# Performance work log

Hardware: AMD Instinct MI355X
Metric: run time of the kernel (lower is better)

## Reference

```python
import jax, jax.numpy as jnp
import numpy as np

NUM_HEADS = 12
DIM = 768


def setup_inputs() -> dict:
    key = jax.random.key(0)
    ks = jax.random.split(key, 7)
    B, S, E = 8, 1024, DIM
    s = 0.02
    return {
        "x": jax.random.normal(ks[0], (B, S, E), dtype=jnp.float32),
        "Wq": jax.random.normal(ks[1], (E, E), dtype=jnp.float32) * s,
        "bq": jnp.zeros((E,), dtype=jnp.float32),
        "Wk": jax.random.normal(ks[2], (E, E), dtype=jnp.float32) * s,
        "bk": jnp.zeros((E,), dtype=jnp.float32),
        "Wo": jax.random.normal(ks[3], (E, E), dtype=jnp.float32) * s,
        "bo": jnp.zeros((E,), dtype=jnp.float32),
    }


def reference(x, Wq, bq, Wk, bk, Wo, bo):
    B, S, E = x.shape
    n = NUM_HEADS
    d = E // n
    scale = d ** (-0.5)

    def heads(t):  # [B,S,E] -> [B,n,S,d]
        return t.reshape(B, S, n, d).transpose(0, 2, 1, 3)

    q = heads(x @ Wq.T + bq)
    k = heads(x @ Wk.T + bk)
    v = k  # faithful to source bug: v = self.k_w(x)

    attn = jnp.einsum('bnqd,bnkd->bnqk', q, k) * scale  # [B,n,S,S]
    attn = jax.nn.softmax(attn, axis=-1)
    out = jnp.einsum('bnqk,bnkd->bnqd', attn, v)  # [B,n,S,d]
    out = out.transpose(0, 2, 1, 3).reshape(B, S, E)
    return out @ Wo.T + bo
```

## Files before the change

### kernel.cpp

```cpp
#include <hip/hip_runtime.h>
#include <stdint.h>


using short8   = __attribute__((ext_vector_type(8))) short;
using uint4v   = __attribute__((ext_vector_type(4))) unsigned;
using float4v  = __attribute__((ext_vector_type(4))) float;
using float16v = __attribute__((ext_vector_type(16))) float;

struct __align__(8) U2 { unsigned x, y; };

__device__ __forceinline__ void async16(void* lds, const void* g) {
  __builtin_amdgcn_global_load_lds(
      (const __attribute__((address_space(1))) void*)g,
      (__attribute__((address_space(3))) void*)lds, 16, 0, 0);
}

#define LGKM_WAIT  asm volatile("s_waitcnt lgkmcnt(0)" ::: "memory")
#define BARRIER    asm volatile("s_barrier" ::: "memory")

__device__ __forceinline__ unsigned bf16b(float f) {
  union { float f; unsigned u; } v; v.f = f;
  unsigned r = v.u + 0x7FFFu + ((v.u >> 16) & 1u);
  return r >> 16;
}
__device__ __forceinline__ unsigned rne_adj(float f) {
  union { float f; unsigned u; } v; v.f = f;
  return v.u + 0x7FFFu + ((v.u >> 16) & 1u);
}
__device__ __forceinline__ unsigned pack_hi16(unsigned a, unsigned b) {
  return __builtin_amdgcn_perm(a, b, 0x07060302u);
}

__global__ __launch_bounds__(256) void cvt_bf16(const float* __restrict__ in,
                                                unsigned short* __restrict__ out,
                                                int n8) {
  int i = blockIdx.x * 256 + threadIdx.x;
  if (i >= n8) return;
  const float4v* p = (const float4v*)in;
  float4v a = p[i * 2], b = p[i * 2 + 1];
  uint4v w;
  w[0] = pack_hi16(rne_adj(a[1]), rne_adj(a[0]));
  w[1] = pack_hi16(rne_adj(a[3]), rne_adj(a[2]));
  w[2] = pack_hi16(rne_adj(b[1]), rne_adj(b[0]));
  w[3] = pack_hi16(rne_adj(b[3]), rne_adj(b[2]));
  ((uint4v*)out)[i] = w;
}

__global__ __launch_bounds__(256) void cvt_w3(const float* __restrict__ w0,
                                              const float* __restrict__ w1,
                                              const float* __restrict__ w2,
                                              unsigned short* __restrict__ o0,
                                              unsigned short* __restrict__ o1,
                                              unsigned short* __restrict__ o2) {
  int mi = blockIdx.x / 288;
  int i = (blockIdx.x - mi * 288) * 256 + threadIdx.x;
  const float* in = (mi == 0) ? w0 : (mi == 1) ? w1 : w2;
  unsigned short* out = (mi == 0) ? o0 : (mi == 1) ? o1 : o2;
  const float4v* p = (const float4v*)in;
  float4v a = p[i * 2], b = p[i * 2 + 1];
  uint4v w;
  w[0] = pack_hi16(rne_adj(a[1]), rne_adj(a[0]));
  w[1] = pack_hi16(rne_adj(a[3]), rne_adj(a[2]));
  w[2] = pack_hi16(rne_adj(b[1]), rne_adj(b[0]));
  w[3] = pack_hi16(rne_adj(b[3]), rne_adj(b[2]));
  ((uint4v*)out)[i] = w;
}

__global__ __launch_bounds__(256, 3) void sgemm_qk(
    const unsigned short* __restrict__ A, const unsigned short* __restrict__ B,
    const float* __restrict__ bias0, const float* __restrict__ bias1,
    unsigned short* __restrict__ outq, unsigned short* __restrict__ outk,
    unsigned short* __restrict__ outkt) {
  __shared__ __align__(16) unsigned short a_l[8192];
  __shared__ __align__(16) unsigned short b_l[8192];
  const int tid = threadIdx.x;
  const int w = tid >> 6, lane = tid & 63;
  const int Q4 = lane >> 4, r = lane & 15;
  const int m0 = blockIdx.x * 128;
  const int n0 = blockIdx.y * 128;
  const int wm = w >> 1, wn = w & 1;

  float4v acc[4][4];
#pragma unroll
  for (int i = 0; i < 4; ++i)
#pragma unroll
    for (int j = 0; j < 4; ++j)
#pragma unroll
      for (int g = 0; g < 4; ++g) acc[i][j][g] = 0.0f;

  const unsigned short* Ab = A + (size_t)(m0 + r) * 768 + Q4 * 8;
  const unsigned short* Bb = B + (size_t)(n0 + r) * 768 + Q4 * 8;

  uint4v ra[4], rb[4];
  auto gload = [&](int kt) {
#pragma unroll
    for (int ci = 0; ci < 4; ++ci) {
      int idx = w * 4 + ci, c = idx >> 1, kh = idx & 1;
      ra[ci] = *(const uint4v*)(Ab + c * 12288 + kt + kh * 32);
      rb[ci] = *(const uint4v*)(Bb + c * 12288 + kt + kh * 32);
    }
  };
  auto swrite = [&]() {
#pragma unroll
    for (int ci = 0; ci < 4; ++ci) {
      int idx = w * 4 + ci;
      *(uint4v*)&a_l[idx * 512 + lane * 8] = ra[ci];
      *(uint4v*)&b_l[idx * 512 + lane * 8] = rb[ci];
    }
  };

  short8 af[4][2], bf[4][2];
  auto loadf = [&]() {
#pragma unroll
    for (int i = 0; i < 4; ++i)
#pragma unroll
      for (int ks = 0; ks < 2; ++ks) {
        af[i][ks] = *(const short8*)&a_l[((wm * 4 + i) * 2 + ks) * 512 + lane * 8];
        bf[i][ks] = *(const short8*)&b_l[((wn * 4 + i) * 2 + ks) * 512 + lane * 8];
      }
  };
  auto dot = [&]() {
#pragma unroll
    for (int mt = 0; mt < 4; ++mt)
#pragma unroll
      for (int nt = 0; nt < 4; ++nt)
#pragma unroll
        for (int ks = 0; ks < 2; ++ks)
          acc[mt][nt] = __builtin_amdgcn_mfma_f32_16x16x32_bf16(
              af[mt][ks], bf[nt][ks], acc[mt][nt], 0, 0, 0);
  };

  gload(0);
#pragma unroll 1
  for (int t = 0; t < 12; ++t) {
    if (t > 0) BARRIER;
    swrite();
    if (t < 11) gload(t * 64 + 64);
    LGKM_WAIT;
    BARRIER;
    loadf();
    dot();
  }

  const bool isq = (n0 < 768);
  const float* bias = isq ? bias0 : bias1;
  unsigned short* outp = isq ? outq : outk;
  const int nb = isq ? n0 : (n0 - 768);
  const float scl = isq ? 0.18033688011112042f : 1.0f;
#pragma unroll
  for (int nt = 0; nt < 4; ++nt) {
    int n = nb + wn * 64 + nt * 16 + r;
    float bv = bias[n];
#pragma unroll
    for (int mt = 0; mt < 4; ++mt) {
      int m = m0 + wm * 64 + mt * 16 + Q4 * 4;
#pragma unroll
      for (int g = 0; g < 4; ++g)
        outp[(size_t)(m + g) * 768 + n] = (unsigned short)bf16b((acc[mt][nt][g] + bv) * scl);
    }
  }
  if (!isq) {
    const int bq = m0 >> 10;
    const int sbase = (m0 & 1023) + wm * 64 + (Q4 & 1) * 8 + (Q4 >> 1) * 4;
#pragma unroll
    for (int nt = 0; nt < 4; ++nt) {
      int n = nb + wn * 64 + nt * 16 + r;
      int hh = n >> 6, dd = n & 63;
      float bv = bias[n];
#pragma unroll
      for (int mt = 0; mt < 4; ++mt) {
        int ns = sbase + mt * 16;
        unsigned lo = pack_hi16(rne_adj(acc[mt][nt][1] + bv), rne_adj(acc[mt][nt][0] + bv));
        unsigned hi = pack_hi16(rne_adj(acc[mt][nt][3] + bv), rne_adj(acc[mt][nt][2] + bv));
        *(U2*)(outkt + (size_t)((bq * 12 + hh) * 64 + dd) * 1024 + ns) = U2{lo, hi};
      }
    }
  }
}

__global__ __launch_bounds__(256, 3) void sgemm_out(
    const unsigned short* __restrict__ A, const unsigned short* __restrict__ B,
    const float* __restrict__ bias, float* __restrict__ outp) {
  __shared__ __align__(16) unsigned short a_l[4096];
  __shared__ __align__(16) unsigned short b_l[8192];
  const int tid = threadIdx.x;
  const int w = tid >> 6, lane = tid & 63;
  const int Q4 = lane >> 4, r = lane & 15;
  const int m0 = blockIdx.y * 64;
  const int n0 = blockIdx.x * 128;
  const int wm = w >> 1, wn = w & 1;

  float4v acc[2][4];
#pragma unroll
  for (int i = 0; i < 2; ++i)
#pragma unroll
    for (int j = 0; j < 4; ++j)
#pragma unroll
      for (int g = 0; g < 4; ++g) acc[i][j][g] = 0.0f;

  const unsigned short* Ab = A + (size_t)(m0 + r) * 768 + Q4 * 8;
  const unsigned short* Bb = B + (size_t)(n0 + r) * 768 + Q4 * 8;

  uint4v ra[2], rb[4];
  auto gload = [&](int kt) {
#pragma unroll
    for (int ci = 0; ci < 2; ++ci) {
      int idx = w * 2 + ci;
      ra[ci] = *(const uint4v*)(Ab + (idx >> 1) * 12288 + kt + (idx & 1) * 32);
    }
#pragma unroll
    for (int ci = 0; ci < 4; ++ci) {
      int idx = w * 4 + ci;
      rb[ci] = *(const uint4v*)(Bb + (idx >> 1) * 12288 + kt + (idx & 1) * 32);
    }
  };
  auto swrite = [&]() {
#pragma unroll
    for (int ci = 0; ci < 2; ++ci) {
      int idx = w * 2 + ci;
      *(uint4v*)&a_l[idx * 512 + lane * 8] = ra[ci];
    }
#pragma unroll
    for (int ci = 0; ci < 4; ++ci) {
      int idx = w * 4 + ci;
      *(uint4v*)&b_l[idx * 512 + lane * 8] = rb[ci];
    }
  };

  short8 af[2][2], bf[4][2];
  auto loadf = [&]() {
#pragma unroll
    for (int i = 0; i < 2; ++i)
#pragma unroll
      for (int ks = 0; ks < 2; ++ks)
        af[i][ks] = *(const short8*)&a_l[((wm * 2 + i) * 2 + ks) * 512 + lane * 8];
#pragma unroll
    for (int i = 0; i < 4; ++i)
#pragma unroll
      for (int ks = 0; ks < 2; ++ks)
        bf[i][ks] = *(const short8*)&b_l[((wn * 4 + i) * 2 + ks) * 512 + lane * 8];
  };
  auto dot = [&]() {
#pragma unroll
    for (int mt = 0; mt < 2; ++mt)
#pragma unroll
      for (int nt = 0; nt < 4; ++nt)
#pragma unroll
        for (int ks = 0; ks < 2; ++ks)
          acc[mt][nt] = __builtin_amdgcn_mfma_f32_16x16x32_bf16(
              af[mt][ks], bf[nt][ks], acc[mt][nt], 0, 0, 0);
  };

  gload(0);
#pragma unroll 1
  for (int t = 0; t < 12; ++t) {
    if (t > 0) BARRIER;
    swrite();
    if (t < 11) gload(t * 64 + 64);
    LGKM_WAIT;
    BARRIER;
    loadf();
    dot();
  }

#pragma unroll
  for (int nt = 0; nt < 4; ++nt) {
    int n = n0 + wn * 64 + nt * 16 + r;
    float bv = bias[n];
#pragma unroll
    for (int mt = 0; mt < 2; ++mt) {
      int m = m0 + wm * 32 + mt * 16 + Q4 * 4;
#pragma unroll
      for (int g = 0; g < 4; ++g)
        outp[(size_t)(m + g) * 768 + n] = acc[mt][nt][g] + bv;
    }
  }
}

__global__ __launch_bounds__(256, 3) void attn_fused(
    const unsigned short* __restrict__ qg,
    const unsigned short* __restrict__ kg,
    const unsigned short* __restrict__ ktg,
    unsigned short* __restrict__ ao) {
  __shared__ __align__(16) unsigned short q_l[8192];
  __shared__ __align__(16) unsigned short k_l[8192];
  __shared__ __align__(16) unsigned short vt_l[8192];

  const int tid = threadIdx.x;
  const int w = tid >> 6, lane = tid & 63;
  const int l31 = lane & 31, hi = lane >> 5;
  const int bid = blockIdx.x;
  const int b = bid & 7;
  const int h = bid >> 6;
  const int qt = (bid >> 3) & 7;
  const int q0 = qt * 128;
  const int bh = b * 12 + h;

#pragma unroll
  for (int ci = 0; ci < 4; ++ci) {
    int c = w * 4 + ci;
    async16(&q_l[c * 512 + lane * 8],
            qg + ((size_t)(b * 1024 + q0 + (c >> 2) * 32 + l31) * 768 + h * 64 + (c & 3) * 16 + hi * 8));
    async16(&k_l[c * 512 + lane * 8],
            kg + ((size_t)(b * 1024 + (c >> 2) * 32 + l31) * 768 + h * 64 + (c & 3) * 16 + hi * 8));
    async16(&vt_l[c * 512 + lane * 8],
            ktg + ((size_t)(bh * 64 + (c >> 3) * 32 + l31) * 1024 + (c & 7) * 16 + hi * 8));
  }
  __syncthreads();

  short8 bfq[4];
#pragma unroll
  for (int kb = 0; kb < 4; ++kb)
    bfq[kb] = *(const short8*)&q_l[(w * 4 + kb) * 512 + lane * 8];

  float16v o_acc[2];
#pragma unroll
  for (int db = 0; db < 2; ++db)
#pragma unroll
    for (int e = 0; e < 16; ++e) o_acc[db][e] = 0.0f;
  float ps = 0.0f;

#pragma unroll 1
  for (int it = 0; it < 8; ++it) {
    if (it > 0) {
      const int s0 = it * 128;
      __syncthreads();
#pragma unroll
      for (int ci = 0; ci < 4; ++ci) {
        int c = w * 4 + ci;
        async16(&k_l[c * 512 + lane * 8],
                kg + ((size_t)(b * 1024 + s0 + (c >> 2) * 32 + l31) * 768 + h * 64 + (c & 3) * 16 + hi * 8));
        async16(&vt_l[c * 512 + lane * 8],
                ktg + ((size_t)(bh * 64 + (c >> 3) * 32 + l31) * 1024 + s0 + (c & 7) * 16 + hi * 8));
      }
      __syncthreads();
    }

    float16v sc[4];
#pragma unroll
    for (int sb = 0; sb < 4; ++sb)
#pragma unroll
      for (int e = 0; e < 16; ++e) sc[sb][e] = 0.0f;
#pragma unroll
    for (int sb = 0; sb < 4; ++sb)
#pragma unroll
      for (int kb = 0; kb < 4; ++kb) {
        short8 af = *(const short8*)&k_l[(sb * 4 + kb) * 512 + lane * 8];
        sc[sb] = __builtin_amdgcn_mfma_f32_32x32x16_bf16(af, bfq[kb], sc[sb], 0, 0, 0);
      }

#pragma unroll
    for (int sb = 0; sb < 4; ++sb) {
      float pe[16];
#pragma unroll
      for (int e = 0; e < 16; ++e) pe[e] = __builtin_amdgcn_exp2f(sc[sb][e]);
#pragma unroll
      for (int e = 0; e < 16; ++e) ps += pe[e];
      uint4v w0, w1;
#pragma unroll
      for (int p = 0; p < 4; ++p) {
        w0[p] = pack_hi16(rne_adj(pe[2 * p + 1]), rne_adj(pe[2 * p]));
        w1[p] = pack_hi16(rne_adj(pe[2 * p + 9]), rne_adj(pe[2 * p + 8]));
      }
      short8 pf0 = __builtin_bit_cast(short8, w0);
      short8 pf1 = __builtin_bit_cast(short8, w1);
#pragma unroll
      for (int db = 0; db < 2; ++db) {
        short8 vf0 = *(const short8*)&vt_l[(db * 8 + sb * 2) * 512 + lane * 8];
        o_acc[db] = __builtin_amdgcn_mfma_f32_32x32x16_bf16(vf0, pf0, o_acc[db], 0, 0, 0);
        short8 vf1 = *(const short8*)&vt_l[(db * 8 + sb * 2 + 1) * 512 + lane * 8];
        o_acc[db] = __builtin_amdgcn_mfma_f32_32x32x16_bf16(vf1, pf1, o_acc[db], 0, 0, 0);
      }
    }
  }

  ps += __shfl_xor(ps, 32, 64);
  const float inv = 1.0f / ps;
  const size_t rowbase = (size_t)(b * 1024 + q0 + w * 32 + l31) * 768 + h * 64;
#pragma unroll
  for (int db = 0; db < 2; ++db)
#pragma unroll
    for (int qq = 0; qq < 4; ++qq) {
      unsigned lo = pack_hi16(rne_adj(o_acc[db][qq * 4 + 1] * inv),
                              rne_adj(o_acc[db][qq * 4 + 0] * inv));
      unsigned hh = pack_hi16(rne_adj(o_acc[db][qq * 4 + 3] * inv),
                              rne_adj(o_acc[db][qq * 4 + 2] * inv));
      *(U2*)(ao + rowbase + db * 32 + qq * 8 + hi * 4) = U2{lo, hh};
    }
}

extern "C" void kernel_launch(void* const* d_in, const int* in_sizes, int n_in,
                              void* d_out, int out_size, void* d_ws, size_t ws_size,
                              hipStream_t stream) {
  const float* x  = (const float*)d_in[0];
  const float* Wq = (const float*)d_in[1];
  const float* bq = (const float*)d_in[2];
  const float* Wk = (const float*)d_in[3];
  const float* bk = (const float*)d_in[4];
  const float* Wo = (const float*)d_in[5];
  const float* bo = (const float*)d_in[6];
  (void)in_sizes; (void)n_in; (void)out_size; (void)ws_size;

  char* ws = (char*)d_ws;
  unsigned short* x_b   = (unsigned short*)(ws);
  unsigned short* wqk_b = (unsigned short*)(ws + 12582912);
  unsigned short* wo_b  = (unsigned short*)(ws + 14942208);
  unsigned short* q_b   = (unsigned short*)(ws + 16121856);
  unsigned short* k_b   = (unsigned short*)(ws + 28704768);
  unsigned short* kt_b  = (unsigned short*)(ws + 41287680);
  unsigned short* ao_b  = (unsigned short*)(ws + 53870592);

  cvt_bf16<<<3072, 256, 0, stream>>>(x, x_b, 786432);
  cvt_w3<<<864, 256, 0, stream>>>(Wq, Wk, Wo, wqk_b, wqk_b + 589824, wo_b);

  sgemm_qk<<<dim3(64, 12), 256, 0, stream>>>(x_b, wqk_b, bq, bk, q_b, k_b, kt_b);
  attn_fused<<<768, 256, 0, stream>>>(q_b, k_b, kt_b, ao_b);
  sgemm_out<<<dim3(6, 128), 256, 0, stream>>>(ao_b, wo_b, bo, (float*)d_out);
}
```

Measured before the change: 199.2 us.

## Rewrite QK projection GEMM as 256x256 tile, 8-wave, async double-buffered pipeline

Replaces the 128x128 register-staged QK projection GEMM with a 512-thread kernel that computes 256x256 tiles. Global-to-LDS async loads fill a double-buffered 128KB LDS with XOR-swizzled addresses, and the loads are interleaved across four MFMA quadrant phases using setprio and explicit vmcnt waits. The block index is remapped for locality across 192 workgroups. The aim is to hide global latency, avoid the register round trip and raise data reuse per tile. In exchange it uses a lot of LDS, so occupancy is low, and it launches 192 blocks, which may underfill the CUs.

```diff
diff --git a/kernel.cpp b/kernel.cpp
--- a/kernel.cpp
+++ b/kernel.cpp
@@ -17,6 +17,11 @@
 
 #define LGKM_WAIT  asm volatile("s_waitcnt lgkmcnt(0)" ::: "memory")
 #define BARRIER    asm volatile("s_barrier" ::: "memory")
+
+template <int N> __device__ __forceinline__ void vm_wait() {
+  if constexpr (N == 4) asm volatile("s_waitcnt vmcnt(4)" ::: "memory");
+  else if constexpr (N == 0) asm volatile("s_waitcnt vmcnt(0)" ::: "memory");
+}
 
 __device__ __forceinline__ unsigned bf16b(float f) {
   union { float f; unsigned u; } v; v.f = f;
@@ -66,81 +71,122 @@
   ((uint4v*)out)[i] = w;
 }
 
-__global__ __launch_bounds__(256, 3) void sgemm_qk(
+template <int BUF, int WAIT, class F1, class F2, class F3, class F4>
+__device__ __forceinline__ void ktile4(const char* lds, int aoff, int boff,
+                                       float4v (&acc)[2][2][2][4],
+                                       F1&& s1, F2&& s2, F3&& s3, F4&& s4) {
+  constexpr int AB = BUF * 65536;
+  constexpr int BB = BUF * 65536 + 32768;
+  short8 af[2][2], b0[4][2], b1[4][2];
+
+#define RD_A(MH)                                                              \
+  _Pragma("unroll") for (int mf = 0; mf < 2; ++mf)                            \
+  _Pragma("unroll") for (int ks = 0; ks < 2; ++ks)                            \
+    af[mf][ks] = *(const short8*)(lds + AB + (MH)*16384 + aoff + mf*2048 + ks*64);
+#define RD_B(NH, BF)                                                          \
+  _Pragma("unroll") for (int nf = 0; nf < 4; ++nf)                            \
+  _Pragma("unroll") for (int ks = 0; ks < 2; ++ks)                            \
+    BF[nf][ks] = *(const short8*)(lds + BB + (NH)*16384 + boff + nf*2048 + ks*64);
+#define MM(MH, NH, BF)                                                        \
+  _Pragma("unroll") for (int mf = 0; mf < 2; ++mf)                            \
+  _Pragma("unroll") for (int nf = 0; nf < 4; ++nf)                            \
+  _Pragma("unroll") for (int ks = 0; ks < 2; ++ks)                            \
+    acc[MH][NH][mf][nf] = __builtin_amdgcn_mfma_f32_16x16x32_bf16(            \
+        af[mf][ks], BF[nf][ks], acc[MH][NH][mf][nf], 0, 0, 0);
+
+  RD_A(0) RD_B(0, b0) s1();
+  BARRIER; LGKM_WAIT; __builtin_amdgcn_sched_barrier(0);
+  __builtin_amdgcn_s_setprio(1); MM(0, 0, b0) __builtin_amdgcn_s_setprio(0);
+  BARRIER;
+  RD_B(1, b1) s2();
+  BARRIER; LGKM_WAIT; __builtin_amdgcn_sched_barrier(0);
+  __builtin_amdgcn_s_setprio(1); MM(0, 1, b1) __builtin_amdgcn_s_setprio(0);
+  BARRIER;
+  RD_A(1) s3();
+  BARRIER; LGKM_WAIT; __builtin_amdgcn_sched_barrier(0);
+  __builtin_amdgcn_s_setprio(1); MM(1, 1, b1) __builtin_amdgcn_s_setprio(0);
+  BARRIER;
+  s4();
+  BARRIER; LGKM_WAIT; __builtin_amdgcn_sched_barrier(0);
+  __builtin_amdgcn_s_setprio(1); MM(1, 0, b0) __builtin_amdgcn_s_setprio(0);
+  vm_wait<WAIT>();
+  BARRIER;
+#undef RD_A
+#undef RD_B
+#undef MM
+}
+
+__global__ __launch_bounds__(512, 2) void sgemm_qk8(
     const unsigned short* __restrict__ A, const unsigned short* __restrict__ B,
     const float* __restrict__ bias0, const float* __restrict__ bias1,
     unsigned short* __restrict__ outq, unsigned short* __restrict__ outk,
     unsigned short* __restrict__ outkt) {
-  __shared__ __align__(16) unsigned short a_l[8192];
-  __shared__ __align__(16) unsigned short b_l[8192];
+  extern __shared__ __align__(16) char lds[];
   const int tid = threadIdx.x;
   const int w = tid >> 6, lane = tid & 63;
   const int Q4 = lane >> 4, r = lane & 15;
-  const int m0 = blockIdx.x * 128;
-  const int n0 = blockIdx.y * 128;
-  const int wm = w >> 1, wn = w & 1;
-
-  float4v acc[4][4];
-#pragma unroll
-  for (int i = 0; i < 4; ++i)
-#pragma unroll
-    for (int j = 0; j < 4; ++j)
-#pragma unroll
-      for (int g = 0; g < 4; ++g) acc[i][j][g] = 0.0f;
-
-  const unsigned short* Ab = A + (size_t)(m0 + r) * 768 + Q4 * 8;
-  const unsigned short* Bb = B + (size_t)(n0 + r) * 768 + Q4 * 8;
-
-  uint4v ra[4], rb[4];
-  auto gload = [&](int kt) {
-#pragma unroll
-    for (int ci = 0; ci < 4; ++ci) {
-      int idx = w * 4 + ci, c = idx >> 1, kh = idx & 1;
-      ra[ci] = *(const uint4v*)(Ab + c * 12288 + kt + kh * 32);
-      rb[ci] = *(const uint4v*)(Bb + c * 12288 + kt + kh * 32);
-    }
-  };
-  auto swrite = [&]() {
-#pragma unroll
-    for (int ci = 0; ci < 4; ++ci) {
-      int idx = w * 4 + ci;
-      *(uint4v*)&a_l[idx * 512 + lane * 8] = ra[ci];
-      *(uint4v*)&b_l[idx * 512 + lane * 8] = rb[ci];
-    }
-  };
-
-  short8 af[4][2], bf[4][2];
-  auto loadf = [&]() {
-#pragma unroll
-    for (int i = 0; i < 4; ++i)
-#pragma unroll
-      for (int ks = 0; ks < 2; ++ks) {
-        af[i][ks] = *(const short8*)&a_l[((wm * 4 + i) * 2 + ks) * 512 + lane * 8];
-        bf[i][ks] = *(const short8*)&b_l[((wn * 4 + i) * 2 + ks) * 512 + lane * 8];
-      }
-  };
-  auto dot = [&]() {
-#pragma unroll
-    for (int mt = 0; mt < 4; ++mt)
-#pragma unroll
-      for (int nt = 0; nt < 4; ++nt)
-#pragma unroll
-        for (int ks = 0; ks < 2; ++ks)
-          acc[mt][nt] = __builtin_amdgcn_mfma_f32_16x16x32_bf16(
-              af[mt][ks], bf[nt][ks], acc[mt][nt], 0, 0, 0);
-  };
-
-  gload(0);
+  const int wr = w & 3, wc = w >> 2;
+  const int bid = blockIdx.x;
+  const int wg = (bid & 7) * 24 + (bid >> 3);
+  const int m0 = (wg / 6) * 256;
+  const int n0 = (wg % 6) * 256;
+
+  const int srow = lane >> 3;
+  const int scol = ((lane & 7) * 8) ^ ((lane >> 5) * 16);
+
+  auto stA = [&](int buf, int half, int t) {
+#pragma unroll
+    for (int j = 0; j < 2; ++j)
+      async16(lds + buf * 65536 + half * 16384 + (w * 2 + j) * 1024 + lane * 16,
+              A + (size_t)(m0 + half * 128 + (w * 2 + j) * 8 + srow) * 768 +
+                  t * 64 + scol);
+  };
+  auto stB = [&](int buf, int half, int t) {
+#pragma unroll
+    for (int j = 0; j < 2; ++j)
+      async16(lds + buf * 65536 + 32768 + half * 16384 + (w * 2 + j) * 1024 + lane * 16,
+              B + (size_t)(n0 + half * 128 + (w * 2 + j) * 8 + srow) * 768 +
+                  t * 64 + scol);
+  };
+
+  const int flip = ((lane >> 2) & 1) * 32;
+  const int aoff = (wr * 32 + r) * 128 + ((Q4 * 16) ^ flip);
+  const int boff = (wc * 64 + r) * 128 + ((Q4 * 16) ^ flip);
+
+  float4v acc[2][2][2][4];
+#pragma unroll
+  for (int a = 0; a < 2; ++a)
+#pragma unroll
+    for (int b = 0; b < 2; ++b)
+#pragma unroll
+      for (int c = 0; c < 2; ++c)
+#pragma unroll
+        for (int d = 0; d < 4; ++d)
+#pragma unroll
+          for (int g = 0; g < 4; ++g) acc[a][b][c][d][g] = 0.0f;
+
+  stA(0, 0, 0); stB(0, 0, 0); stB(0, 1, 0); stA(0, 1, 0);
+  stA(1, 0, 1); stB(1, 1, 1);
+  vm_wait<4>(); BARRIER;
+
 #pragma unroll 1
-  for (int t = 0; t < 12; ++t) {
-    if (t > 0) BARRIER;
-    swrite();
-    if (t < 11) gload(t * 64 + 64);
-    LGKM_WAIT;
-    BARRIER;
-    loadf();
-    dot();
-  }
+  for (int i = 0; i < 5; ++i) {
+    const int t1 = 2 * i + 1, t2 = 2 * i + 2, t3 = 2 * i + 3;
+    ktile4<0, 4>(lds, aoff, boff, acc,
+                 [&] { stA(1, 1, t1); stB(1, 0, t1); },
+                 [&] {},
+                 [&] { stA(0, 0, t2); },
+                 [&] { stB(0, 1, t2); });
+    ktile4<1, 4>(lds, aoff, boff, acc,
+                 [&] { stA(0, 1, t2); stB(0, 0, t2); },
+                 [&] {},
+                 [&] { stA(1, 0, t3); },
+                 [&] { stB(1, 1, t3); });
+  }
+  ktile4<0, 0>(lds, aoff, boff, acc,
+               [&] { stA(1, 1, 11); stB(1, 0, 11); },
+               [&] {}, [&] {}, [&] {});
+  ktile4<1, -1>(lds, aoff, boff, acc, [&] {}, [&] {}, [&] {}, [&] {});
 
   const bool isq = (n0 < 768);
   const float* bias = isq ? bias0 : bias1;
@@ -148,33 +194,44 @@
   const int nb = isq ? n0 : (n0 - 768);
   const float scl = isq ? 0.18033688011112042f : 1.0f;
 #pragma unroll
-  for (int nt = 0; nt < 4; ++nt) {
-    int n = nb + wn * 64 + nt * 16 + r;
-    float bv = bias[n];
-#pragma unroll
-    for (int mt = 0; mt < 4; ++mt) {
-      int m = m0 + wm * 64 + mt * 16 + Q4 * 4;
-#pragma unroll
-      for (int g = 0; g < 4; ++g)
-        outp[(size_t)(m + g) * 768 + n] = (unsigned short)bf16b((acc[mt][nt][g] + bv) * scl);
-    }
-  }
+  for (int Nh = 0; Nh < 2; ++Nh)
+#pragma unroll
+    for (int nf = 0; nf < 4; ++nf) {
+      const int n = nb + Nh * 128 + wc * 64 + nf * 16 + r;
+      const float bv = bias[n];
+#pragma unroll
+      for (int Mh = 0; Mh < 2; ++Mh)
+#pragma unroll
+        for (int mf = 0; mf < 2; ++mf) {
+          const int m = m0 + Mh * 128 + wr * 32 + mf * 16 + Q4 * 4;
+#pragma unroll
+          for (int g = 0; g < 4; ++g)
+            outp[(size_t)(m + g) * 768 + n] =
+                (unsigned short)bf16b((acc[Mh][Nh][mf][nf][g] + bv) * scl);
+        }
+    }
   if (!isq) {
     const int bq = m0 >> 10;
-    const int sbase = (m0 & 1023) + wm * 64 + (Q4 & 1) * 8 + (Q4 >> 1) * 4;
-#pragma unroll
-    for (int nt = 0; nt < 4; ++nt) {
-      int n = nb + wn * 64 + nt * 16 + r;
-      int hh = n >> 6, dd = n & 63;
-      float bv = bias[n];
-#pragma unroll
-      for (int mt = 0; mt < 4; ++mt) {
-        int ns = sbase + mt * 16;
-        unsigned lo = pack_hi16(rne_adj(acc[mt][nt][1] + bv), rne_adj(acc[mt][nt][0] + bv));
-        unsigned hi = pack_hi16(rne_adj(acc[mt][nt][3] + bv), rne_adj(acc[mt][nt][2] + bv));
-        *(U2*)(outkt + (size_t)((bq * 12 + hh) * 64 + dd) * 1024 + ns) = U2{lo, hi};
+    const int sb0 = (m0 & 1023) + wr * 32 + (Q4 & 1) * 8 + (Q4 >> 1) * 4;
+#pragma unroll
+    for (int Nh = 0; Nh < 2; ++Nh)
+#pragma unroll
+      for (int nf = 0; nf < 4; ++nf) {
+        const int nk = nb + Nh * 128 + wc * 64 + nf * 16 + r;
+        const int hh = nk >> 6, dd = nk & 63;
+        const float bv = bias1[nk];
+#pragma unroll
+        for (int Mh = 0; Mh < 2; ++Mh)
+#pragma unroll
+          for (int mf = 0; mf < 2; ++mf) {
+            const int ns = sb0 + Mh * 128 + mf * 16;
+            const float4v a4 = acc[Mh][Nh][mf][nf];
+            unsigned lo = pack_hi16(rne_adj(a4[1] + bv), rne_adj(a4[0] + bv));
+            unsigned hi = pack_hi16(rne_adj(a4[3] + bv), rne_adj(a4[2] + bv));
+            *(U2*)(outkt + (size_t)((bq * 12 + hh) * 64 + dd) * 1024 + ns) =
+                U2{lo, hi};
+          }
       }
-    }
   }
 }
 
@@ -401,6 +458,13 @@
   const float* bo = (const float*)d_in[6];
   (void)in_sizes; (void)n_in; (void)out_size; (void)ws_size;
 
+  static bool inited = false;
+  if (!inited) {
+    (void)hipFuncSetAttribute((const void*)sgemm_qk8,
+                              hipFuncAttributeMaxDynamicSharedMemorySize, 131072);
+    inited = true;
+  }
+
   char* ws = (char*)d_ws;
   unsigned short* x_b   = (unsigned short*)(ws);
   unsigned short* wqk_b = (unsigned short*)(ws + 12582912);
@@ -413,7 +477,7 @@
   cvt_bf16<<<3072, 256, 0, stream>>>(x, x_b, 786432);
   cvt_w3<<<864, 256, 0, stream>>>(Wq, Wk, Wo, wqk_b, wqk_b + 589824, wo_b);
 
-  sgemm_qk<<<dim3(64, 12), 256, 0, stream>>>(x_b, wqk_b, bq, bk, q_b, k_b, kt_b);
+  sgemm_qk8<<<192, 512, 131072, stream>>>(x_b, wqk_b, bq, bk, q_b, k_b, kt_b);
   attn_fused<<<768, 256, 0, stream>>>(q_b, k_b, kt_b, ao_b);
   sgemm_out<<<dim3(6, 128), 256, 0, stream>>>(ao_b, wo_b, bo, (float*)d_out);
 }
```

Measured after the change: 196.0 us. About the same (-1.6%).
